# Kernel optimization log

Hardware: AMD Instinct MI355X
Metric: run time of the kernel (lower is better)

Reference implementation:

```python
import jax, jax.numpy as jnp
import numpy as np

SOFTASSIGN_LAYERS = 10  # MTSPSoftassign layers
EPS = 1e-8


def softassign(output):
    # output: (b, m, n, n)
    b, m, n, _ = output.shape
    # stabilizing max-subtraction (layers > 0 branch)
    depots_max = jnp.max(output[:, :, :1, :], axis=3, keepdims=True)            # (b,m,1,1)
    others_max = jnp.max(output[:, :, 1:, :], axis=(1, 3), keepdims=True)       # (b,1,n-1,1)
    output_max = jnp.concatenate([
        jnp.broadcast_to(depots_max, (b, m, 1, n)),
        jnp.broadcast_to(others_max, (b, m, n - 1, n)),
    ], axis=2)
    output = jnp.exp(output - output_max)
    for _ in range(SOFTASSIGN_LAYERS):
        output = jnp.maximum(output, EPS)
        starts = output[:, :, :1, :]
        starts = starts / jnp.sum(starts, axis=3, keepdims=True)                # normalize_dims (3,)
        nexts = output[:, :, 1:, :]
        nexts = nexts / jnp.sum(nexts, axis=(1, 3), keepdims=True)              # normalize_dims (1,3)
        output = jnp.swapaxes(jnp.concatenate([starts, nexts], axis=2), 2, 3)
    if SOFTASSIGN_LAYERS % 2 != 0:
        output = jnp.swapaxes(output, 2, 3)
    return output


def setup_inputs() -> dict:
    key = jax.random.key(0)
    ks = jax.random.split(key, 4)
    b, m, n, d = 4, 8, 128, 64
    cities = jax.random.normal(ks[0], (b, n, d), dtype=jnp.float32)
    groups = jax.random.normal(ks[1], (b, m, d), dtype=jnp.float32)
    W1 = jax.random.normal(ks[2], (3 * d, d), dtype=jnp.float32) * 0.05
    b1 = jnp.zeros((d,), dtype=jnp.float32)
    W2 = jax.random.normal(ks[3], (d, 1), dtype=jnp.float32) * 0.05
    b2 = jnp.zeros((1,), dtype=jnp.float32)
    return {"cities": cities, "groups": groups, "W1": W1, "b1": b1, "W2": W2, "b2": b2}


def reference(cities, groups, W1, b1, W2, b2):
    # cities: (b, n, d) embedded city features; groups: (b, m, d) embedded group features.
    # Torch builds nodes = cat(at_groups, from_cities, to_cities) of shape (b,m,n,n,3d)
    # then Linear(3d->d). Linear on a concat == sum of linears on the pieces, so we
    # project each piece once and broadcast-add, avoiding the (b,m,n,n,3d) materialization.
    d = cities.shape[-1]
    Wg, Wf, Wt = W1[:d], W1[d:2 * d], W1[2 * d:]
    hg = jnp.einsum('bmd,de->bme', groups, Wg)   # at_groups projection
    hf = jnp.einsum('bnd,de->bne', cities, Wf)   # from_cities projection
    ht = jnp.einsum('bnd,de->bne', cities, Wt)   # to_cities projection
    h = hg[:, :, None, None, :] + hf[:, None, :, None, :] + ht[:, None, None, :, :] + b1  # (b,m,n,n,d)
    h = jax.nn.relu(h)
    out = jnp.einsum('bmfte,eo->bmfto', h, W2)[..., 0] + b2[0]  # (b,m,n,n)
    return softassign(out)
```

## Files before the change

kernel.cpp:

```cpp
#include <hip/hip_runtime.h>
#include <math.h>

#define EPSF 1e-8f

__device__ __forceinline__ void atomicMaxFloat(float* addr, float val) {
    if (val >= 0.f) atomicMax((int*)addr, __float_as_int(val));
    else            atomicMin((unsigned int*)addr, __float_as_uint(val));
}

__global__ __launch_bounds__(256) void prep_kernel(
        const float* __restrict__ cities, const float* __restrict__ groups,
        const float* __restrict__ W1,
        float* __restrict__ hg, float* __restrict__ hf, float* __restrict__ htT,
        float* __restrict__ S, float* __restrict__ Mbuf,
        unsigned* __restrict__ cnt) {
    int blk = blockIdx.x, tid = threadIdx.x;
    if (blk < 128) {
        int gid = blk * 256 + tid;
        int e = gid & 63;
        int f = (gid >> 6) & 127;
        int b = gid >> 13;
        const float* crow = cities + (b * 128 + f) * 64;
        float af = 0.f, at = 0.f;
        #pragma unroll 8
        for (int d = 0; d < 64; ++d) {
            float c = crow[d];
            af = fmaf(c, W1[(64  + d) * 64 + e], af);
            at = fmaf(c, W1[(128 + d) * 64 + e], at);
        }
        hf [(b * 128 + f) * 64 + e] = af;
        htT[(b * 64  + e) * 128 + f] = at;
    } else if (blk < 136) {
        int gid = (blk - 128) * 256 + tid;
        int e = gid & 63;
        int m = (gid >> 6) & 7;
        int b = gid >> 9;
        const float* grow = groups + (b * 8 + m) * 64;
        float a = 0.f;
        #pragma unroll 8
        for (int d = 0; d < 64; ++d)
            a = fmaf(grow[d], W1[d * 64 + e], a);
        hg[(b * 8 + m) * 64 + e] = a;
    } else {
        for (int i = tid; i < 5120; i += 256) S[i] = 0.f;
        for (int i = tid; i < 544;  i += 256) Mbuf[i] = -INFINITY;
        if (tid < 40) cnt[tid] = 0u;
    }
}

__global__ __launch_bounds__(128) void mlp_kernel(
        const float* __restrict__ hg, const float* __restrict__ hf,
        const float* __restrict__ htT,
        const float* __restrict__ b1, const float* __restrict__ W2,
        const float* __restrict__ b2,
        float* __restrict__ X, float* __restrict__ Mdep, float* __restrict__ Moth) {
    int r = blockIdx.x;
    int f = r & 127, m = (r >> 7) & 7, b = r >> 10;
    int t = threadIdx.x;
    __shared__ float arow[64], w2s[64];
    if (t < 64) {
        arow[t] = hg[(b * 8 + m) * 64 + t] + hf[(b * 128 + f) * 64 + t] + b1[t];
        w2s[t]  = W2[t];
    }
    __syncthreads();
    const float* htb = htT + b * 8192;
    float acc = 0.f;
    #pragma unroll 16
    for (int e = 0; e < 64; ++e) {
        float v = arow[e] + htb[e * 128 + t];
        acc = fmaf(fmaxf(v, 0.f), w2s[e], acc);
    }
    float out = acc + b2[0];
    X[r * 128 + t] = out;

    float mx = out;
    #pragma unroll
    for (int off = 32; off; off >>= 1) mx = fmaxf(mx, __shfl_down(mx, off));
    __shared__ float wm[2];
    if ((t & 63) == 0) wm[t >> 6] = mx;
    __syncthreads();
    if (t == 0) {
        float bm = fmaxf(wm[0], wm[1]);
        if (f == 0) atomicMaxFloat(&Mdep[b * 8 + m], bm);
        else        atomicMaxFloat(&Moth[b * 128 + f], bm);
    }
}

__global__ __launch_bounds__(1024) void softassign_kernel(
        float* __restrict__ X, const float* __restrict__ Mdep,
        const float* __restrict__ Moth, float* __restrict__ S,
        unsigned* __restrict__ cnt) {
    int blk = blockIdx.x;
    int b = blk >> 3;
    int tid = threadIdx.x;
    int tf = tid >> 5, tt = tid & 31;
    float* base = X + blk * 16384;

    float x[4][4];
    #pragma unroll
    for (int r = 0; r < 4; ++r) {
        float4 v = *(const float4*)(base + (4 * tf + r) * 128 + 4 * tt);
        x[r][0] = v.x; x[r][1] = v.y; x[r][2] = v.z; x[r][3] = v.w;
    }

    float mdep = Mdep[blk];
    #pragma unroll
    for (int r = 0; r < 4; ++r) {
        int f = 4 * tf + r;
        float M = (f == 0) ? mdep : Moth[b * 128 + f];
        #pragma unroll
        for (int c = 0; c < 4; ++c) x[r][c] = expf(x[r][c] - M);
    }

    __shared__ float part[128][33];
    __shared__ float dnm[128];
    __shared__ float depot;

    for (int k = 0; k < 10; ++k) {
        #pragma unroll
        for (int r = 0; r < 4; ++r)
            #pragma unroll
            for (int c = 0; c < 4; ++c) x[r][c] = fmaxf(x[r][c], EPSF);

        int dir = k & 1;
        if (dir == 0) {
            #pragma unroll
            for (int r = 0; r < 4; ++r)
                part[4 * tf + r][tt] = x[r][0] + x[r][1] + x[r][2] + x[r][3];
        } else {
            #pragma unroll
            for (int c = 0; c < 4; ++c)
                part[4 * tt + c][tf] = x[0][c] + x[1][c] + x[2][c] + x[3][c];
        }
        __syncthreads();
        float* Scur = &S[(k * 4 + b) * 128];
        if (tid < 128) {
            float s = 0.f;
            #pragma unroll 8
            for (int j = 0; j < 32; ++j) s += part[tid][j];
            if (tid == 0) depot = s;
            else atomicAdd(&Scur[tid], s);
        }
        __syncthreads();
        unsigned* ccur = &cnt[k * 4 + b];
        if (tid == 0) {
            __hip_atomic_fetch_add(ccur, 1u, __ATOMIC_RELAXED,
                                   __HIP_MEMORY_SCOPE_AGENT);
            while (__hip_atomic_load(ccur, __ATOMIC_RELAXED,
                                     __HIP_MEMORY_SCOPE_AGENT) < 8u)
                __builtin_amdgcn_s_sleep(1);
        }
        __syncthreads();

        if (tid < 128) {
            dnm[tid] = (tid == 0) ? depot
                : __hip_atomic_load(&Scur[tid], __ATOMIC_RELAXED,
                                    __HIP_MEMORY_SCOPE_AGENT);
        }
        __syncthreads();

        if (dir == 0) {
            #pragma unroll
            for (int r = 0; r < 4; ++r) {
                float inv = 1.f / dnm[4 * tf + r];
                #pragma unroll
                for (int c = 0; c < 4; ++c) x[r][c] *= inv;
            }
        } else {
            #pragma unroll
            for (int c = 0; c < 4; ++c) {
                float inv = 1.f / dnm[4 * tt + c];
                #pragma unroll
                for (int r = 0; r < 4; ++r) x[r][c] *= inv;
            }
        }
    }

    #pragma unroll
    for (int r = 0; r < 4; ++r) {
        float4 v = make_float4(x[r][0], x[r][1], x[r][2], x[r][3]);
        *(float4*)(base + (4 * tf + r) * 128 + 4 * tt) = v;
    }
}

extern "C" void kernel_launch(void* const* d_in, const int* in_sizes, int n_in,
                              void* d_out, int out_size, void* d_ws, size_t ws_size,
                              hipStream_t stream) {
    const float* cities = (const float*)d_in[0];
    const float* groups = (const float*)d_in[1];
    const float* W1     = (const float*)d_in[2];
    const float* b1     = (const float*)d_in[3];
    const float* W2     = (const float*)d_in[4];
    const float* b2     = (const float*)d_in[5];
    float* X  = (float*)d_out;
    float* ws = (float*)d_ws;

    float*    hg   = ws;
    float*    hf   = ws + 2048;
    float*    htT  = ws + 34816;
    float*    S    = ws + 67584;
    float*    Mbuf = ws + 72704;
    float*    Mdep = Mbuf;
    float*    Moth = Mbuf + 32;
    unsigned* cnt  = (unsigned*)(ws + 73248);

    prep_kernel<<<137, 256, 0, stream>>>(cities, groups, W1, hg, hf, htT,
                                         S, Mbuf, cnt);
    mlp_kernel<<<4096, 128, 0, stream>>>(hg, hf, htT, b1, W2, b2, X, Mdep, Moth);
    softassign_kernel<<<32, 1024, 0, stream>>>(X, Mdep, Moth, S, cnt);
}
```

Baseline: 105.6 us.

## Tile MLP kernel over 8 from-rows per block with ht staged in LDS

Restructures the MLP kernel so each 256-thread block handles 8 from-city rows for one (b,m) instead of one row per 128-thread block. The full per-batch ht^T slice (32KB) is copied into shared memory and reused across rows, and each thread accumulates 4 outputs, reusing each ht value from a register. The goal is to cut redundant global loads of ht and per-block launch and atomic overhead. The cost is a 32KB LDS footprint per block, which may limit occupancy, and fewer blocks (512) in the grid.

```diff
diff --git a/kernel.cpp b/kernel.cpp
--- a/kernel.cpp
+++ b/kernel.cpp
@@ -48,41 +48,80 @@
     }
 }
 
-__global__ __launch_bounds__(128) void mlp_kernel(
+__global__ __launch_bounds__(256) void mlp_kernel(
         const float* __restrict__ hg, const float* __restrict__ hf,
         const float* __restrict__ htT,
         const float* __restrict__ b1, const float* __restrict__ W2,
         const float* __restrict__ b2,
         float* __restrict__ X, float* __restrict__ Mdep, float* __restrict__ Moth) {
-    int r = blockIdx.x;
-    int f = r & 127, m = (r >> 7) & 7, b = r >> 10;
-    int t = threadIdx.x;
-    __shared__ float arow[64], w2s[64];
-    if (t < 64) {
-        arow[t] = hg[(b * 8 + m) * 64 + t] + hf[(b * 128 + f) * 64 + t] + b1[t];
-        w2s[t]  = W2[t];
-    }
+    int blk = blockIdx.x;
+    int fg  = blk & 15;
+    int bm  = blk >> 4;
+    int b   = bm >> 3;
+    int tid = threadIdx.x;
+
+    __shared__ float hts[64][128];
+    __shared__ float arowT[64][8];
+    __shared__ float w2s[64];
+    __shared__ float wmax[4][4];
+
+    {
+        const float4* src = (const float4*)(htT + b * 8192);
+        float4* dst = (float4*)(&hts[0][0]);
+        #pragma unroll
+        for (int i = 0; i < 8; ++i) dst[tid + 256 * i] = src[tid + 256 * i];
+    }
+    #pragma unroll
+    for (int j = 0; j < 2; ++j) {
+        int v = tid + 256 * j;
+        int e = v >> 3, f8 = v & 7;
+        int f = fg * 8 + f8;
+        arowT[e][f8] = hg[bm * 64 + e] + hf[(b * 128 + f) * 64 + e] + b1[e];
+    }
+    if (tid < 64) w2s[tid] = W2[tid];
     __syncthreads();
-    const float* htb = htT + b * 8192;
-    float acc = 0.f;
-    #pragma unroll 16
+
+    int t  = tid & 127;
+    int fo = tid >> 7;
+    float acc[4] = {0.f, 0.f, 0.f, 0.f};
+    #pragma unroll 8
     for (int e = 0; e < 64; ++e) {
-        float v = arow[e] + htb[e * 128 + t];
-        acc = fmaf(fmaxf(v, 0.f), w2s[e], acc);
-    }
-    float out = acc + b2[0];
-    X[r * 128 + t] = out;
-
-    float mx = out;
-    #pragma unroll
-    for (int off = 32; off; off >>= 1) mx = fmaxf(mx, __shfl_down(mx, off));
-    __shared__ float wm[2];
-    if ((t & 63) == 0) wm[t >> 6] = mx;
+        float ht = hts[e][t];
+        float w2 = w2s[e];
+        float4 ar = *(const float4*)(&arowT[e][fo * 4]);
+        acc[0] = fmaf(fmaxf(ar.x + ht, 0.f), w2, acc[0]);
+        acc[1] = fmaf(fmaxf(ar.y + ht, 0.f), w2, acc[1]);
+        acc[2] = fmaf(fmaxf(ar.z + ht, 0.f), w2, acc[2]);
+        acc[3] = fmaf(fmaxf(ar.w + ht, 0.f), w2, acc[3]);
+    }
+
+    float b2v = b2[0];
+    float fmax4[4];
+    #pragma unroll
+    for (int i = 0; i < 4; ++i) {
+        float out = acc[i] + b2v;
+        int f = fg * 8 + fo * 4 + i;
+        X[(bm * 128 + f) * 128 + t] = out;
+        fmax4[i] = out;
+    }
+
+    #pragma unroll
+    for (int i = 0; i < 4; ++i)
+        #pragma unroll
+        for (int off = 32; off; off >>= 1)
+            fmax4[i] = fmaxf(fmax4[i], __shfl_down(fmax4[i], off));
+    int wv = tid >> 6;
+    if ((tid & 63) == 0) {
+        #pragma unroll
+        for (int i = 0; i < 4; ++i) wmax[wv][i] = fmax4[i];
+    }
     __syncthreads();
-    if (t == 0) {
-        float bm = fmaxf(wm[0], wm[1]);
-        if (f == 0) atomicMaxFloat(&Mdep[b * 8 + m], bm);
-        else        atomicMaxFloat(&Moth[b * 128 + f], bm);
+    if (tid < 8) {
+        int w0 = (tid >> 2) * 2, i = tid & 3;
+        float m = fmaxf(wmax[w0][i], wmax[w0 + 1][i]);
+        int f = fg * 8 + tid;
+        if (f == 0) atomicMaxFloat(&Mdep[bm], m);
+        else        atomicMaxFloat(&Moth[b * 128 + f], m);
     }
 }
 
@@ -206,6 +245,6 @@
 
     prep_kernel<<<137, 256, 0, stream>>>(cities, groups, W1, hg, hf, htT,
                                          S, Mbuf, cnt);
-    mlp_kernel<<<4096, 128, 0, stream>>>(hg, hf, htT, b1, W2, b2, X, Mdep, Moth);
+    mlp_kernel<<<512, 256, 0, stream>>>(hg, hf, htT, b1, W2, b2, X, Mdep, Moth);
     softassign_kernel<<<32, 1024, 0, stream>>>(X, Mdep, Moth, S, cnt);
 }
```

New measurement: 102.7 us. 1.03x faster.
